# Kernel optimization log

Hardware: AMD Instinct MI355X
Metric: run time of the kernel (lower is better)

The kernel has to match this reference:

```python
import jax, jax.numpy as jnp
import numpy as np
from jax import lax

B, L, E = 16, 100, 128
NQ, NC, DL = 1000, 100, 100
NODE, PATH, MAXC = 5000, 5000, 128


def setup_inputs() -> dict:
    key = jax.random.key(0)
    ks = jax.random.split(key, 40)
    rn = lambda k, *s: jax.random.normal(k, s, jnp.float32) * 0.02
    inp = {}
    inp['code'] = jax.random.randint(ks[0], (B, L, NQ * 2 + MAXC * 3), 0, NODE, jnp.int32)
    inp['q'] = jax.random.randint(ks[1], (B, L), 0, NQ, jnp.int32)
    inp['c'] = jax.random.randint(ks[2], (B, L), 0, NC, jnp.int32)
    inp['sd'] = jax.random.randint(ks[3], (B, L), 0, DL, jnp.int32)
    inp['qd'] = jax.random.randint(ks[4], (B, L), 0, DL, jnp.int32)
    inp['a'] = jax.random.randint(ks[5], (B, L), 0, NQ * 2, jnp.int32)
    inp['qshft'] = jax.random.randint(ks[6], (B, L), 0, NQ, jnp.int32)
    inp['cshft'] = jax.random.randint(ks[7], (B, L), 0, NC, jnp.int32)
    inp['sdshft'] = jax.random.randint(ks[8], (B, L), 0, DL, jnp.int32)
    inp['qdshft'] = jax.random.randint(ks[9], (B, L), 0, DL, jnp.int32)
    # embedding tables (padding rows zeroed, matching torch padding_idx)
    inp['embed_nodes'] = rn(ks[10], NODE + 2, E)
    inp['embed_paths'] = rn(ks[11], PATH + 2, E)
    inp['q_tab'] = rn(ks[12], NQ + 1, E).at[NQ].set(0.0)
    inp['c_tab'] = rn(ks[13], NC + 1, E).at[NC].set(0.0)
    inp['sd_tab'] = rn(ks[14], DL + 100, E).at[0].set(0.0)
    inp['qd_tab'] = rn(ks[15], DL + 100, E).at[0].set(0.0)
    inp['a_tab'] = rn(ks[16], NQ * 2 + 2, E).at[2].set(0.0)
    inp['knowledge'] = rn(ks[17], 1, E)
    # linear weights stored [in, out] so y = x @ W + b
    inp['Wpt'] = rn(ks[18], 3 * E, 3 * E); inp['bpt'] = rn(ks[19], 3 * E)
    inp['Wat'] = rn(ks[20], 3 * E, 1);     inp['bat'] = rn(ks[21], 1)
    inp['Wqa'] = rn(ks[22], 4 * E, E);     inp['bqa'] = rn(ks[23], E)
    inp['W1'] = rn(ks[24], 4 * E, E);      inp['b1'] = rn(ks[25], E)
    inp['W2'] = rn(ks[26], E, E);          inp['b2'] = rn(ks[27], E)
    inp['W3'] = rn(ks[28], E, E);          inp['b3'] = rn(ks[29], E)
    inp['W4'] = rn(ks[30], 2 * E, E);      inp['b4'] = rn(ks[31], E)
    inp['W5'] = rn(ks[32], 2 * E, E);      inp['b5'] = rn(ks[33], E)
    inp['W6'] = rn(ks[34], 4 * E, E);      inp['b6'] = rn(ks[35], E)
    inp['Wf'] = rn(ks[36], E, 10);         inp['bf'] = rn(ks[37], 10)
    return inp


def reference(code, q, c, sd, qd, a, qshft, cshft, sdshft, qdshft,
              embed_nodes, embed_paths, q_tab, c_tab, sd_tab, qd_tab, a_tab,
              knowledge, Wpt, bpt, Wat, bat, Wqa, bqa, W1, b1, W2, b2, W3, b3,
              W4, b4, W5, b5, W6, b6, Wf, bf):
    Bq, Lq = q.shape
    # ---- code2vec attention over AST paths ----
    c2v = code[:, :, NQ * 2:].reshape(Bq, Lq, MAXC, 3)
    full = jnp.concatenate([embed_nodes[c2v[..., 0]],
                            embed_nodes[c2v[..., 2]],
                            embed_paths[c2v[..., 1]]], axis=-1)  # [B,L,MAXC,3E]
    tr = jnp.tanh(full @ Wpt + bpt)
    ctx = tr @ Wat + bat                      # [B,L,MAXC,1]
    attn = jax.nn.softmax(ctx, axis=1)        # softmax over seq dim (dim=1), as in source
    code_vec = jnp.sum(full * attn, axis=2)   # [B,L,3E]
    # ---- embeddings + input projections ----
    a_e = a_tab[a]
    acode = jnp.concatenate([a_e, code_vec], axis=-1) @ Wqa + bqa   # [B,L,E]
    inp = jnp.concatenate([q_tab[q], c_tab[c], sd_tab[sd], qd_tab[qd]], axis=-1) @ W1 + b1
    sd_e = sd_tab[sd]
    qd_e = qd_tab[qd]
    # ---- sequential SDF/PKA/KSU recurrence ----
    k0 = jnp.tile(knowledge, (Bq, 1))  # [B,E]

    def step(k, ts):
        inp_t, a_t, sd_t, qd_t = ts
        qq = inp_t - k
        sdf = jax.nn.sigmoid(qq @ W2 + b2) * jnp.tanh(qq @ W3 + b3)
        x = jnp.concatenate([sdf, a_t], axis=-1)
        pka = jax.nn.sigmoid(x @ W4 + b4) * jnp.tanh(x @ W5 + b5)
        ins = jnp.concatenate([k, a_t, sd_t, qd_t], axis=-1)
        g = jax.nn.sigmoid(ins @ W6 + b6)
        k_new = g * k + (1.0 - g) * pka
        return k_new, k_new @ Wf + bf

    xs = (inp.transpose(1, 0, 2), acode.transpose(1, 0, 2),
          sd_e.transpose(1, 0, 2), qd_e.transpose(1, 0, 2))
    _, logits = lax.scan(step, k0, xs)        # [L,B,10]
    return jax.nn.sigmoid(logits.transpose(1, 0, 2))  # [B,L,10]
```

## Files before the change

kernel.cpp:

```cpp
#include <hip/hip_runtime.h>
#include <hip/hip_bf16.h>

#define B_   16
#define L_   100
#define E_   128
#define NQ_  1000
#define MAXC_ 128
#define CODE_STRIDE (NQ_*2 + MAXC_*3)
#define CODE_OFF    (NQ_*2)
#define NROWS (B_*L_*MAXC_)

typedef short bf16x8 __attribute__((ext_vector_type(8)));
typedef float f32x4  __attribute__((ext_vector_type(4)));

__device__ __forceinline__ unsigned short f2b(float f) {
    unsigned u = __float_as_uint(f);
    unsigned r = (u + 0x7fffu + ((u >> 16) & 1u)) >> 16;
    return (unsigned short)r;
}
__device__ __forceinline__ unsigned cvt2(float lo, float hi) {
    unsigned r;
    asm("v_cvt_pk_bf16_f32 %0, %1, %2" : "=v"(r) : "v"(lo), "v"(hi));
    return r;
}
__device__ __forceinline__ float fsig(float x) {
    return __builtin_amdgcn_rcpf(1.0f + __builtin_amdgcn_exp2f(-1.44269504f * x));
}
__device__ __forceinline__ float ftanh(float x) {
    return 1.0f - 2.0f * __builtin_amdgcn_rcpf(1.0f + __builtin_amdgcn_exp2f(2.88539008f * x));
}
__device__ __forceinline__ void ldsbar() {
    asm volatile("s_waitcnt lgkmcnt(0)" ::: "memory");
    __builtin_amdgcn_s_barrier();
}
__device__ __forceinline__ void vmbar() {
    asm volatile("s_waitcnt vmcnt(0) lgkmcnt(0)" ::: "memory");
    __builtin_amdgcn_s_barrier();
}
__device__ __forceinline__ void gll16(const void* g, void* l) {
    __builtin_amdgcn_global_load_lds(
        (const __attribute__((address_space(1))) unsigned int*)g,
        (__attribute__((address_space(3))) unsigned int*)l, 16, 0, 0);
}

#define P0 576
#define P1 (P0+2501)
#define P2 (P1+2501)
#define P3 (P2+192)
#define P4 (P3+128)
#define P5 (P4+8)
#define P6 (P5+512)
#define P7 (P6+256)
#define P8 (P7+192)
#define P9 (P8+8)

__global__ void k_prep(const float* __restrict__ Wpt, const float* __restrict__ en,
                       const float* __restrict__ ep,
                       const float* __restrict__ W2, const float* __restrict__ W3,
                       const float* __restrict__ W4, const float* __restrict__ W5,
                       const float* __restrict__ W6, const float* __restrict__ Wf,
                       const float* __restrict__ Wqa, const float* __restrict__ W1,
                       unsigned short* __restrict__ wptT, unsigned short* __restrict__ enb,
                       unsigned short* __restrict__ epb, unsigned short* __restrict__ bt1,
                       unsigned short* __restrict__ bt2, unsigned short* __restrict__ btf,
                       unsigned short* __restrict__ bW1, unsigned short* __restrict__ bW2,
                       unsigned short* __restrict__ bW6, float* __restrict__ ssum)
{
    int blk = blockIdx.x;
    if (blk < P0) {
        int i = blk * 256 + threadIdx.x;
        if (i < 384*384) {
            int e = i & 7, G = i >> 3;
            int l15g = G & 15, rest = G >> 4;
            int l4g = rest & 3, rest2 = rest >> 2;
            int ksg = rest2 % 12, tile = rest2 / 12;
            int n = tile*16 + l15g, k = ksg*32 + l4g*8 + e;
            wptT[i] = f2b(Wpt[k*384 + n]);
        }
    } else if (blk < P1) {
        int i = (blk - P0) * 256 + threadIdx.x;
        if (i < 5002*128) enb[i] = f2b(en[i]);
    } else if (blk < P2) {
        int i = (blk - P1) * 256 + threadIdx.x;
        if (i < 5002*128) epb[i] = f2b(ep[i]);
    } else if (blk < P3) {
        int i = (blk - P2) * 256 + threadIdx.x;
        int n = i >> 7, k = i & 127;
        float v = (n < 128) ? W2[k*128 + n] : (n < 256) ? W3[k*128 + (n-128)]
                                                        : W6[k*128 + (n-256)];
        bt1[i] = f2b(v);
    } else if (blk < P4) {
        int i = (blk - P3) * 256 + threadIdx.x;
        int n = i >> 7, k = i & 127;
        float v = (n < 128) ? W4[k*128 + n] : W5[k*128 + (n-128)];
        bt2[i] = f2b(v);
    } else if (blk < P5) {
        int i = (blk - P4) * 256 + threadIdx.x;
        int n = i >> 7, k = i & 127;
        btf[i] = f2b(n < 10 ? Wf[k*10 + n] : 0.0f);
    } else if (blk < P6) {
        int i = (blk - P5) * 256 + threadIdx.x;
        int n = i >> 9, k = i & 511;
        float v = (n < 128) ? Wqa[k*128 + n] : W1[k*128 + (n-128)];
        bW1[i] = f2b(v);
    } else if (blk < P7) {
        int i = (blk - P6) * 256 + threadIdx.x;
        int n = i >> 7, k = i & 127;
        float v = (n < 128) ? W2[k*128 + n]
                : (n < 256) ? W3[k*128 + (n-128)]
                : (n < 384) ? W4[(128 + k)*128 + (n-256)]
                            : W5[(128 + k)*128 + (n-384)];
        bW2[i] = f2b(v);
    } else if (blk < P8) {
        int i = (blk - P7) * 256 + threadIdx.x;
        if (i < 128*384) {
            int n = i / 384, k = i % 384;
            bW6[i] = f2b(W6[(128 + k)*128 + n]);
        }
    } else {
        int i = (blk - P8) * 256 + threadIdx.x;
        if (i < B_ * MAXC_) ssum[i] = 0.0f;
    }
}

__global__ __launch_bounds__(256, 2) void k_ctx(const int* __restrict__ code,
    const unsigned short* __restrict__ enb, const unsigned short* __restrict__ epb,
    const unsigned short* __restrict__ wptT, const float* __restrict__ bpt,
    const float* __restrict__ wat, const float* __restrict__ bat,
    float* __restrict__ ectx, float* __restrict__ ssum)
{
    __shared__ __align__(16) unsigned short Bs[2][18432];
    __shared__ float bw[768];
    const int tid = threadIdx.x, wv = tid >> 6, lane = tid & 63;
    const int l15 = lane & 15, l4 = lane >> 4;
    const int rowg0 = blockIdx.x * 192;

    for (int idx = tid; idx < 768; idx += 256)
        bw[idx] = (idx < 384) ? bpt[idx] : wat[idx - 384];

    bf16x8 af[3][12];
    #pragma unroll
    for (int h = 0; h < 3; ++h) {
        int rowg = rowg0 + h * 64 + wv * 16 + l15;
        int rowc = (rowg < NROWS) ? rowg : (NROWS - 1);
        int m = rowc & 127, bl = rowc >> 7;
        const int* cp = code + (size_t)bl * CODE_STRIDE + CODE_OFF + m * 3;
        int i0 = cp[0], i1 = cp[1], i2 = cp[2];
        #pragma unroll
        for (int ks = 0; ks < 12; ++ks) {
            int seg = ks >> 2;
            int idx = (seg == 0) ? i0 : (seg == 1 ? i2 : i1);
            const unsigned short* tab = (seg == 2) ? epb : enb;
            af[h][ks] = *(const bf16x8*)(tab + (size_t)idx * 128 + (ks & 3) * 32 + l4 * 8);
        }
    }

    {
        const unsigned short* src = wptT;
        #pragma unroll
        for (int i = 0; i < 9; ++i) {
            int g0 = wv * 64 + i * 256;
            gll16(src + (size_t)g0 * 8 + lane * 8, &Bs[0][g0 * 8]);
        }
    }

    float cr[3][4] = {{0,0,0,0},{0,0,0,0},{0,0,0,0}};
    const float bat0 = bat[0];

    for (int nc = 0; nc < 8; ++nc) {
        vmbar();
        if (nc < 7) {
            const unsigned short* src = wptT + (size_t)(nc + 1) * 18432;
            #pragma unroll
            for (int i = 0; i < 9; ++i) {
                int g0 = wv * 64 + i * 256;
                gll16(src + (size_t)g0 * 8 + lane * 8, &Bs[(nc + 1) & 1][g0 * 8]);
            }
        }
        const char* bb = (const char*)&Bs[nc & 1][0] + l15 * 16;
        f32x4 acc[3][3] = {{{0,0,0,0},{0,0,0,0},{0,0,0,0}},
                           {{0,0,0,0},{0,0,0,0},{0,0,0,0}},
                           {{0,0,0,0},{0,0,0,0},{0,0,0,0}}};
        #pragma unroll
        for (int ks = 0; ks < 12; ++ks) {
            int go = (ks * 4 + l4) * 256;
            bf16x8 b0 = *(const bf16x8*)(bb + go);
            bf16x8 b1 = *(const bf16x8*)(bb + 24576 + go);
            bf16x8 b2 = *(const bf16x8*)(bb + 49152 + go);
            #pragma unroll
            for (int h = 0; h < 3; ++h) {
                acc[h][0] = __builtin_amdgcn_mfma_f32_16x16x32_bf16(af[h][ks], b0, acc[h][0], 0, 0, 0);
                acc[h][1] = __builtin_amdgcn_mfma_f32_16x16x32_bf16(af[h][ks], b1, acc[h][1], 0, 0, 0);
                acc[h][2] = __builtin_amdgcn_mfma_f32_16x16x32_bf16(af[h][ks], b2, acc[h][2], 0, 0, 0);
            }
        }
        #pragma unroll
        for (int tt = 0; tt < 3; ++tt) {
            int ng = nc * 48 + tt * 16 + l15;
            float bv = bw[ng], wa = bw[384 + ng];
            #pragma unroll
            for (int h = 0; h < 3; ++h)
                #pragma unroll
                for (int r = 0; r < 4; ++r)
                    cr[h][r] += ftanh(acc[h][tt][r] + bv) * wa;
        }
    }

    #pragma unroll
    for (int h = 0; h < 3; ++h)
        #pragma unroll
        for (int r = 0; r < 4; ++r) {
            float v = cr[h][r];
            v += __shfl_xor(v, 1); v += __shfl_xor(v, 2);
            v += __shfl_xor(v, 4); v += __shfl_xor(v, 8);
            cr[h][r] = v;
        }
    if (l15 == 0) {
        #pragma unroll
        for (int h = 0; h < 3; ++h) {
            int rbase = rowg0 + h * 64 + wv * 16 + l4 * 4;
            #pragma unroll
            for (int r = 0; r < 4; ++r) {
                int row = rbase + r;
                if (row < NROWS) {
                    float e = __builtin_amdgcn_exp2f((cr[h][r] + bat0) * 1.44269504f);
                    ectx[row] = e;
                    int bl = row >> 7, m = row & 127;
                    atomicAdd(&ssum[(bl / 100) * 128 + m], e);
                }
            }
        }
    }
}

__global__ __launch_bounds__(192) void k_codevec(const int* __restrict__ code,
    const float* __restrict__ ectx, const float* __restrict__ ssum,
    const unsigned short* __restrict__ enb, const unsigned short* __restrict__ epb,
    float* __restrict__ cv)
{
    __shared__ float sm[128];
    int bl = blockIdx.x;
    int t = threadIdx.x;
    if (t < 128) {
        sm[t] = ectx[(size_t)bl * MAXC_ + t]
                * __builtin_amdgcn_rcpf(ssum[(bl / 100) * 128 + t]);
    }
    ldsbar();
    int seg = t >> 6, tc = t & 63;
    const int* cp = code + (size_t)bl * CODE_STRIDE + CODE_OFF;
    const unsigned short* tab = (seg == 2) ? epb : enb;
    const int sidx = (seg == 0) ? 0 : (seg == 1) ? 2 : 1;
    float ax = 0.f, ay = 0.f;
    #pragma unroll 8
    for (int m = 0; m < MAXC_; ++m) {
        float w = sm[m];
        int idx = cp[m * 3 + sidx];
        unsigned u = *((const unsigned*)(tab + (size_t)idx * 128) + tc);
        ax += w * __uint_as_float(u << 16);
        ay += w * __uint_as_float(u & 0xffff0000u);
    }
    float2 o; o.x = ax; o.y = ay;
    *(float2*)(cv + (size_t)bl * 384 + seg * 128 + tc * 2) = o;
}

__global__ __launch_bounds__(256) void k_fuse(
    const int* __restrict__ a, const int* __restrict__ q, const int* __restrict__ c,
    const int* __restrict__ sd, const int* __restrict__ qd,
    const float* __restrict__ a_tab, const float* __restrict__ q_tab,
    const float* __restrict__ c_tab, const float* __restrict__ sd_tab,
    const float* __restrict__ qd_tab, const float* __restrict__ cv,
    const unsigned short* __restrict__ bW1, const unsigned short* __restrict__ bW2,
    const unsigned short* __restrict__ bW6,
    const float* __restrict__ bqa, const float* __restrict__ b1,
    const float* __restrict__ b2, const float* __restrict__ b3,
    const float* __restrict__ b4, const float* __restrict__ b5,
    const float* __restrict__ b6,
    float4* __restrict__ preQ, float* __restrict__ pre6)
{
    __shared__ __align__(16) unsigned short X[16 * 1024];
    __shared__ __align__(16) unsigned short Y[16 * 256];
    const int tid = threadIdx.x, wv = tid >> 6, lane = tid & 63;
    const int l15 = lane & 15, l4 = lane >> 4;
    const int row0 = blockIdx.x * 16;

    #pragma unroll
    for (int it = 0; it < 16; ++it) {
        int idx = tid + it * 256;
        int r = idx >> 8, col = (idx & 255) * 4;
        int row = row0 + r;
        const float* src;
        if (col < 128)       src = a_tab + (size_t)a[row] * 128 + col;
        else if (col < 512)  src = cv + (size_t)row * 384 + (col - 128);
        else if (col < 640)  src = q_tab + (size_t)q[row] * 128 + (col - 512);
        else if (col < 768)  src = c_tab + (size_t)c[row] * 128 + (col - 640);
        else if (col < 896)  src = sd_tab + (size_t)sd[row] * 128 + (col - 768);
        else                 src = qd_tab + (size_t)qd[row] * 128 + (col - 896);
        float4 v = *(const float4*)src;
        unsigned u0 = cvt2(v.x, v.y), u1 = cvt2(v.z, v.w);
        int byte = r * 2048 + ((((col >> 3)) ^ (r & 7)) << 4) + ((col & 4) << 1);
        *(unsigned*)((char*)X + byte) = u0;
        *(unsigned*)((char*)X + byte + 4) = u1;
    }
    ldsbar();

    {
        bf16x8 ak[16];
        int kbase = (wv < 2) ? 0 : 512;
        #pragma unroll
        for (int ks = 0; ks < 16; ++ks) {
            int col = kbase + ks * 32 + l4 * 8;
            ak[ks] = *(const bf16x8*)((const char*)X + l15 * 2048 + (((col >> 3) ^ (l15 & 7)) << 4));
        }
        int nbase = wv * 64;
        f32x4 acc[4] = {{0,0,0,0},{0,0,0,0},{0,0,0,0},{0,0,0,0}};
        #pragma unroll
        for (int i = 0; i < 4; ++i) {
            const unsigned short* bp = bW1 + (size_t)(nbase + i * 16 + l15) * 512 + l4 * 8;
            #pragma unroll
            for (int ks = 0; ks < 16; ++ks) {
                bf16x8 bfr = *(const bf16x8*)(bp + ks * 32);
                acc[i] = __builtin_amdgcn_mfma_f32_16x16x32_bf16(ak[ks], bfr, acc[i], 0, 0, 0);
            }
        }
        #pragma unroll
        for (int i = 0; i < 4; ++i) {
            int cc = nbase + i * 16 + l15;
            float bias = (cc < 128) ? bqa[cc] : b1[cc - 128];
            #pragma unroll
            for (int rr = 0; rr < 4; ++rr) {
                int row = l4 * 4 + rr;
                int byte = row * 512 + (((cc >> 3) ^ (row & 7)) << 4) + (cc & 7) * 2;
                *(unsigned short*)((char*)Y + byte) = f2b(acc[i][rr] + bias);
            }
        }
    }
    ldsbar();

    bf16x8 zi[4], za[4], zs[4], zq[4];
    #pragma unroll
    for (int ks = 0; ks < 4; ++ks) {
        int ci = 128 + ks * 32 + l4 * 8;
        zi[ks] = *(const bf16x8*)((const char*)Y + l15 * 512 + (((ci >> 3) ^ (l15 & 7)) << 4));
        int ca = ks * 32 + l4 * 8;
        za[ks] = *(const bf16x8*)((const char*)Y + l15 * 512 + (((ca >> 3) ^ (l15 & 7)) << 4));
        int cs = 768 + ks * 32 + l4 * 8;
        zs[ks] = *(const bf16x8*)((const char*)X + l15 * 2048 + (((cs >> 3) ^ (l15 & 7)) << 4));
        int cq = 896 + ks * 32 + l4 * 8;
        zq[ks] = *(const bf16x8*)((const char*)X + l15 * 2048 + (((cq >> 3) ^ (l15 & 7)) << 4));
    }
    f32x4 A2[2] = {{0,0,0,0},{0,0,0,0}}, A3[2] = {{0,0,0,0},{0,0,0,0}};
    f32x4 A4[2] = {{0,0,0,0},{0,0,0,0}}, A5[2] = {{0,0,0,0},{0,0,0,0}};
    f32x4 A6[2] = {{0,0,0,0},{0,0,0,0}};
    #pragma unroll
    for (int tt = 0; tt < 2; ++tt) {
        int n = wv * 32 + tt * 16 + l15;
        const unsigned short* p2 = bW2 + (size_t)(      n) * 128 + l4 * 8;
        const unsigned short* p3 = bW2 + (size_t)(128 + n) * 128 + l4 * 8;
        const unsigned short* p4 = bW2 + (size_t)(256 + n) * 128 + l4 * 8;
        const unsigned short* p5 = bW2 + (size_t)(384 + n) * 128 + l4 * 8;
        const unsigned short* p6 = bW6 + (size_t)n * 384 + l4 * 8;
        #pragma unroll
        for (int ks = 0; ks < 4; ++ks) {
            A2[tt] = __builtin_amdgcn_mfma_f32_16x16x32_bf16(zi[ks], *(const bf16x8*)(p2 + ks*32), A2[tt], 0, 0, 0);
            A3[tt] = __builtin_amdgcn_mfma_f32_16x16x32_bf16(zi[ks], *(const bf16x8*)(p3 + ks*32), A3[tt], 0, 0, 0);
            A4[tt] = __builtin_amdgcn_mfma_f32_16x16x32_bf16(za[ks], *(const bf16x8*)(p4 + ks*32), A4[tt], 0, 0, 0);
            A5[tt] = __builtin_amdgcn_mfma_f32_16x16x32_bf16(za[ks], *(const bf16x8*)(p5 + ks*32), A5[tt], 0, 0, 0);
            A6[tt] = __builtin_amdgcn_mfma_f32_16x16x32_bf16(za[ks], *(const bf16x8*)(p6 + ks*32), A6[tt], 0, 0, 0);
        }
        #pragma unroll
        for (int ks = 0; ks < 4; ++ks)
            A6[tt] = __builtin_amdgcn_mfma_f32_16x16x32_bf16(zs[ks], *(const bf16x8*)(p6 + 256 + ks*32), A6[tt], 0, 0, 0);
        #pragma unroll
        for (int ks = 0; ks < 4; ++ks)
            A6[tt] = __builtin_amdgcn_mfma_f32_16x16x32_bf16(zq[ks], *(const bf16x8*)(p6 + 512 + ks*32), A6[tt], 0, 0, 0);
    }
    #pragma unroll
    for (int tt = 0; tt < 2; ++tt) {
        int n = wv * 32 + tt * 16 + l15;
        float c2 = b2[n], c3 = b3[n], c4 = b4[n], c5 = b5[n], c6 = b6[n];
        #pragma unroll
        for (int rr = 0; rr < 4; ++rr) {
            size_t row = (size_t)(row0 + l4 * 4 + rr);
            float4 o;
            o.x = A2[tt][rr] + c2; o.y = A3[tt][rr] + c3;
            o.z = A4[tt][rr] + c4; o.w = A5[tt][rr] + c5;
            preQ[row * 128 + n] = o;
            pre6[row * 128 + n] = A6[tt][rr] + c6;
        }
    }
}

__global__ __launch_bounds__(512) void k_recur(
    const unsigned short* __restrict__ bt1, const unsigned short* __restrict__ bt2,
    const float* __restrict__ knowledge, const float4* __restrict__ preQ,
    const float* __restrict__ pre6, unsigned short* __restrict__ khist)
{
    __shared__ __align__(16) unsigned short k_lds[16 * 128];
    __shared__ __align__(16) unsigned short s_lds[16 * 128];
    const int tid = threadIdx.x, wv = tid >> 6, lane = tid & 63;
    const int l15 = lane & 15, l4 = lane >> 4;
    const int j = wv * 16 + l15;

    bf16x8 w2f[4], w3f[4], w6f[4], w4f[4], w5f[4];
    #pragma unroll
    for (int ks = 0; ks < 4; ++ks) {
        w2f[ks] = *(const bf16x8*)(bt1 + (size_t)(      j) * 128 + ks * 32 + l4 * 8);
        w3f[ks] = *(const bf16x8*)(bt1 + (size_t)(128 + j) * 128 + ks * 32 + l4 * 8);
        w6f[ks] = *(const bf16x8*)(bt1 + (size_t)(256 + j) * 128 + ks * 32 + l4 * 8);
        w4f[ks] = *(const bf16x8*)(bt2 + (size_t)(      j) * 128 + ks * 32 + l4 * 8);
        w5f[ks] = *(const bf16x8*)(bt2 + (size_t)(128 + j) * 128 + ks * 32 + l4 * 8);
    }

    float kreg[4], gR[4];
    {
        float k0 = knowledge[j];
        unsigned short kb = f2b(k0);
        #pragma unroll
        for (int r = 0; r < 4; ++r) {
            kreg[r] = k0;
            int b = l4 * 4 + r;
            k_lds[b * 128 + (((j >> 3) ^ b) << 3) + (j & 7)] = kb;
        }
    }
    ldsbar();

    float4 pv[4]; float p6[4];
    #pragma unroll
    for (int r = 0; r < 4; ++r) {
        int b = l4 * 4 + r;
        size_t ix = (size_t)(b * L_) * 128 + j;
        pv[r] = preQ[ix]; p6[r] = pre6[ix];
    }

    for (int t = 0; t < L_; ++t) {
        float4 pvN[4]; float p6N[4];
        #pragma unroll
        for (int r = 0; r < 4; ++r) {
            int b = l4 * 4 + r;
            size_t ix = (size_t)(b * L_ + t + 1) * 128 + j;
            pvN[r] = preQ[ix]; p6N[r] = pre6[ix];
        }

        bf16x8 ak[4];
        {
            const unsigned short* kb = k_lds + l15 * 128;
            #pragma unroll
            for (int ks = 0; ks < 4; ++ks)
                ak[ks] = *(const bf16x8*)(kb + (((ks * 4 + l4) ^ l15) << 3));
        }
        f32x4 a2 = {0,0,0,0}, a3 = {0,0,0,0}, a6 = {0,0,0,0};
        #pragma unroll
        for (int ks = 0; ks < 4; ++ks) {
            a2 = __builtin_amdgcn_mfma_f32_16x16x32_bf16(ak[ks], w2f[ks], a2, 0, 0, 0);
            a3 = __builtin_amdgcn_mfma_f32_16x16x32_bf16(ak[ks], w3f[ks], a3, 0, 0, 0);
            a6 = __builtin_amdgcn_mfma_f32_16x16x32_bf16(ak[ks], w6f[ks], a6, 0, 0, 0);
        }
        #pragma unroll
        for (int r = 0; r < 4; ++r) {
            int b = l4 * 4 + r;
            float sdf = fsig(pv[r].x - a2[r]) * ftanh(pv[r].y - a3[r]);
            gR[r] = fsig(a6[r] + p6[r]);
            s_lds[b * 128 + (((j >> 3) ^ b) << 3) + (j & 7)] = f2b(sdf);
        }
        ldsbar();
        bf16x8 as[4];
        {
            const unsigned short* sb = s_lds + l15 * 128;
            #pragma unroll
            for (int ks = 0; ks < 4; ++ks)
                as[ks] = *(const bf16x8*)(sb + (((ks * 4 + l4) ^ l15) << 3));
        }
        f32x4 a4 = {0,0,0,0}, a5 = {0,0,0,0};
        #pragma unroll
        for (int ks = 0; ks < 4; ++ks) {
            a4 = __builtin_amdgcn_mfma_f32_16x16x32_bf16(as[ks], w4f[ks], a4, 0, 0, 0);
            a5 = __builtin_amdgcn_mfma_f32_16x16x32_bf16(as[ks], w5f[ks], a5, 0, 0, 0);
        }
        #pragma unroll
        for (int r = 0; r < 4; ++r) {
            int b = l4 * 4 + r;
            float pka = fsig(a4[r] + pv[r].z) * ftanh(a5[r] + pv[r].w);
            float kn = gR[r] * kreg[r] + (1.0f - gR[r]) * pka;
            kreg[r] = kn;
            unsigned short kb2 = f2b(kn);
            k_lds[b * 128 + (((j >> 3) ^ b) << 3) + (j & 7)] = kb2;
            khist[(size_t)(b * L_ + t) * 128 + j] = kb2;
        }
        #pragma unroll
        for (int r = 0; r < 4; ++r) { pv[r] = pvN[r]; p6[r] = p6N[r]; }
        ldsbar();
    }
}

__global__ __launch_bounds__(256) void k_logits(const unsigned short* __restrict__ khist,
    const unsigned short* __restrict__ btf, const float* __restrict__ bfv,
    float* __restrict__ out)
{
    int wv = threadIdx.x >> 6, lane = threadIdx.x & 63;
    int l15 = lane & 15, l4 = lane >> 4;
    int R0 = (blockIdx.x * 4 + wv) * 16;
    bf16x8 wbf[4], akr[4];
    #pragma unroll
    for (int ks = 0; ks < 4; ++ks)
        wbf[ks] = *(const bf16x8*)(btf + (size_t)l15 * 128 + ks * 32 + l4 * 8);
    const unsigned short* kb = khist + (size_t)(R0 + l15) * 128;
    #pragma unroll
    for (int ks = 0; ks < 4; ++ks)
        akr[ks] = *(const bf16x8*)(kb + ks * 32 + l4 * 8);
    f32x4 af = {0.f, 0.f, 0.f, 0.f};
    #pragma unroll
    for (int ks = 0; ks < 4; ++ks)
        af = __builtin_amdgcn_mfma_f32_16x16x32_bf16(akr[ks], wbf[ks], af, 0, 0, 0);
    if (l15 < 10) {
        float bb = bfv[l15];
        #pragma unroll
        for (int r = 0; r < 4; ++r)
            out[(size_t)(R0 + l4 * 4 + r) * 10 + l15] = fsig(af[r] + bb);
    }
}

extern "C" void kernel_launch(void* const* d_in, const int* in_sizes, int n_in,
                              void* d_out, int out_size, void* d_ws, size_t ws_size,
                              hipStream_t stream)
{
    const int*   code  = (const int*)d_in[0];
    const int*   q     = (const int*)d_in[1];
    const int*   c     = (const int*)d_in[2];
    const int*   sd    = (const int*)d_in[3];
    const int*   qd    = (const int*)d_in[4];
    const int*   a     = (const int*)d_in[5];
    const float* en    = (const float*)d_in[10];
    const float* ep    = (const float*)d_in[11];
    const float* q_tab = (const float*)d_in[12];
    const float* c_tab = (const float*)d_in[13];
    const float* sd_tab= (const float*)d_in[14];
    const float* qd_tab= (const float*)d_in[15];
    const float* a_tab = (const float*)d_in[16];
    const float* know  = (const float*)d_in[17];
    const float* Wpt   = (const float*)d_in[18];
    const float* bpt   = (const float*)d_in[19];
    const float* Wat   = (const float*)d_in[20];
    const float* bat   = (const float*)d_in[21];
    const float* Wqa   = (const float*)d_in[22];
    const float* bqa   = (const float*)d_in[23];
    const float* W1    = (const float*)d_in[24];
    const float* b1    = (const float*)d_in[25];
    const float* W2    = (const float*)d_in[26];
    const float* b2    = (const float*)d_in[27];
    const float* W3    = (const float*)d_in[28];
    const float* b3    = (const float*)d_in[29];
    const float* W4    = (const float*)d_in[30];
    const float* b4    = (const float*)d_in[31];
    const float* W5    = (const float*)d_in[32];
    const float* b5    = (const float*)d_in[33];
    const float* W6    = (const float*)d_in[34];
    const float* b6    = (const float*)d_in[35];
    const float* Wf    = (const float*)d_in[36];
    const float* bf_   = (const float*)d_in[37];

    char* ws = (char*)d_ws;
    size_t off = 0;
    auto alloc = [&](size_t n) { size_t r = off; off += (n + 255) & ~(size_t)255; return r; };
    unsigned short* wptT = (unsigned short*)(ws + alloc(384 * 384 * 2));
    unsigned short* enb  = (unsigned short*)(ws + alloc(5002 * 128 * 2));
    unsigned short* epb  = (unsigned short*)(ws + alloc(5002 * 128 * 2));
    unsigned short* bt1  = (unsigned short*)(ws + alloc(384 * 128 * 2));
    unsigned short* bt2  = (unsigned short*)(ws + alloc(256 * 128 * 2));
    unsigned short* btf  = (unsigned short*)(ws + alloc(16 * 128 * 2));
    unsigned short* bW1  = (unsigned short*)(ws + alloc(256 * 512 * 2));
    unsigned short* bW2  = (unsigned short*)(ws + alloc(512 * 128 * 2));
    unsigned short* bW6  = (unsigned short*)(ws + alloc(128 * 384 * 2));
    float* ectx  = (float*)(ws + alloc((size_t)NROWS * 4));
    float* ssum  = (float*)(ws + alloc((size_t)B_ * MAXC_ * 4));
    float* cv    = (float*)(ws + alloc((size_t)B_ * L_ * 384 * 4));
    float4* preQ = (float4*)(ws + alloc(((size_t)B_ * L_ * 128 + 128) * 16));
    float* pre6  = (float*)(ws + alloc(((size_t)B_ * L_ * 128 + 128) * 4));
    unsigned short* khist = (unsigned short*)(ws + alloc((size_t)B_ * L_ * 128 * 2));
    float* outf  = (float*)d_out;

    k_prep<<<P9, 256, 0, stream>>>(Wpt, en, ep, W2, W3, W4, W5, W6, Wf,
                                   Wqa, W1,
                                   wptT, enb, epb, bt1, bt2, btf,
                                   bW1, bW2, bW6, ssum);
    k_ctx<<<1067, 256, 0, stream>>>(code, enb, epb, wptT, bpt, Wat, bat, ectx, ssum);
    k_codevec<<<1600, 192, 0, stream>>>(code, ectx, ssum, enb, epb, cv);
    k_fuse<<<100, 256, 0, stream>>>(a, q, c, sd, qd, a_tab, q_tab, c_tab, sd_tab,
                                    qd_tab, cv, bW1, bW2, bW6, bqa, b1,
                                    b2, b3, b4, b5, b6, preQ, pre6);
    k_recur<<<1, 512, 0, stream>>>(bt1, bt2, know, preQ, pre6, khist);
    k_logits<<<25, 256, 0, stream>>>(khist, btf, bf_, outf);
}
```

Before: 280.9 us.

## Read Wpt B-fragments directly from global in k_ctx, shrink row tile

The k_ctx attention-score kernel drops its LDS double-buffered staging of the transposed Wpt weights (global_load_lds plus barriers) and instead loads B fragments straight from global memory/L2 per MFMA step. The per-block row tile shrinks from 192 to 128 rows (2 row groups per wave instead of 3), so the grid becomes 1600 blocks that divide NROWS exactly, and the bounds checks go away. This removes LDS traffic and barriers and frees LDS for higher occupancy, at the cost of more redundant global/L2 weight reads per block and less reuse of each B fragment.

```diff
diff --git a/kernel.cpp b/kernel.cpp
--- a/kernel.cpp
+++ b/kernel.cpp
@@ -32,15 +32,6 @@
 __device__ __forceinline__ void ldsbar() {
     asm volatile("s_waitcnt lgkmcnt(0)" ::: "memory");
     __builtin_amdgcn_s_barrier();
-}
-__device__ __forceinline__ void vmbar() {
-    asm volatile("s_waitcnt vmcnt(0) lgkmcnt(0)" ::: "memory");
-    __builtin_amdgcn_s_barrier();
-}
-__device__ __forceinline__ void gll16(const void* g, void* l) {
-    __builtin_amdgcn_global_load_lds(
-        (const __attribute__((address_space(1))) unsigned int*)g,
-        (__attribute__((address_space(3))) unsigned int*)l, 16, 0, 0);
 }
 
 #define P0 576
@@ -123,27 +114,21 @@
     }
 }
 
-__global__ __launch_bounds__(256, 2) void k_ctx(const int* __restrict__ code,
+__global__ __launch_bounds__(256) void k_ctx(const int* __restrict__ code,
     const unsigned short* __restrict__ enb, const unsigned short* __restrict__ epb,
     const unsigned short* __restrict__ wptT, const float* __restrict__ bpt,
     const float* __restrict__ wat, const float* __restrict__ bat,
     float* __restrict__ ectx, float* __restrict__ ssum)
 {
-    __shared__ __align__(16) unsigned short Bs[2][18432];
-    __shared__ float bw[768];
     const int tid = threadIdx.x, wv = tid >> 6, lane = tid & 63;
     const int l15 = lane & 15, l4 = lane >> 4;
-    const int rowg0 = blockIdx.x * 192;
-
-    for (int idx = tid; idx < 768; idx += 256)
-        bw[idx] = (idx < 384) ? bpt[idx] : wat[idx - 384];
-
-    bf16x8 af[3][12];
-    #pragma unroll
-    for (int h = 0; h < 3; ++h) {
+    const int rowg0 = blockIdx.x * 128;
+
+    bf16x8 af[2][12];
+    #pragma unroll
+    for (int h = 0; h < 2; ++h) {
         int rowg = rowg0 + h * 64 + wv * 16 + l15;
-        int rowc = (rowg < NROWS) ? rowg : (NROWS - 1);
-        int m = rowc & 127, bl = rowc >> 7;
+        int m = rowg & 127, bl = rowg >> 7;
         const int* cp = code + (size_t)bl * CODE_STRIDE + CODE_OFF + m * 3;
         int i0 = cp[0], i1 = cp[1], i2 = cp[2];
         #pragma unroll
@@ -155,59 +140,30 @@
         }
     }
 
-    {
-        const unsigned short* src = wptT;
-        #pragma unroll
-        for (int i = 0; i < 9; ++i) {
-            int g0 = wv * 64 + i * 256;
-            gll16(src + (size_t)g0 * 8 + lane * 8, &Bs[0][g0 * 8]);
-        }
-    }
-
-    float cr[3][4] = {{0,0,0,0},{0,0,0,0},{0,0,0,0}};
+    float cr[2][4] = {{0.f,0.f,0.f,0.f},{0.f,0.f,0.f,0.f}};
     const float bat0 = bat[0];
-
-    for (int nc = 0; nc < 8; ++nc) {
-        vmbar();
-        if (nc < 7) {
-            const unsigned short* src = wptT + (size_t)(nc + 1) * 18432;
-            #pragma unroll
-            for (int i = 0; i < 9; ++i) {
-                int g0 = wv * 64 + i * 256;
-                gll16(src + (size_t)g0 * 8 + lane * 8, &Bs[(nc + 1) & 1][g0 * 8]);
-            }
-        }
-        const char* bb = (const char*)&Bs[nc & 1][0] + l15 * 16;
-        f32x4 acc[3][3] = {{{0,0,0,0},{0,0,0,0},{0,0,0,0}},
-                           {{0,0,0,0},{0,0,0,0},{0,0,0,0}},
-                           {{0,0,0,0},{0,0,0,0},{0,0,0,0}}};
+    const unsigned short* bbase = wptT + l4 * 128 + l15 * 8;
+
+    for (int t = 0; t < 24; ++t) {
+        const unsigned short* bp = bbase + t * 6144;
+        f32x4 acc0 = {0.f,0.f,0.f,0.f}, acc1 = {0.f,0.f,0.f,0.f};
         #pragma unroll
         for (int ks = 0; ks < 12; ++ks) {
-            int go = (ks * 4 + l4) * 256;
-            bf16x8 b0 = *(const bf16x8*)(bb + go);
-            bf16x8 b1 = *(const bf16x8*)(bb + 24576 + go);
-            bf16x8 b2 = *(const bf16x8*)(bb + 49152 + go);
-            #pragma unroll
-            for (int h = 0; h < 3; ++h) {
-                acc[h][0] = __builtin_amdgcn_mfma_f32_16x16x32_bf16(af[h][ks], b0, acc[h][0], 0, 0, 0);
-                acc[h][1] = __builtin_amdgcn_mfma_f32_16x16x32_bf16(af[h][ks], b1, acc[h][1], 0, 0, 0);
-                acc[h][2] = __builtin_amdgcn_mfma_f32_16x16x32_bf16(af[h][ks], b2, acc[h][2], 0, 0, 0);
-            }
-        }
-        #pragma unroll
-        for (int tt = 0; tt < 3; ++tt) {
-            int ng = nc * 48 + tt * 16 + l15;
-            float bv = bw[ng], wa = bw[384 + ng];
-            #pragma unroll
-            for (int h = 0; h < 3; ++h)
-                #pragma unroll
-                for (int r = 0; r < 4; ++r)
-                    cr[h][r] += ftanh(acc[h][tt][r] + bv) * wa;
-        }
-    }
-
-    #pragma unroll
-    for (int h = 0; h < 3; ++h)
+            bf16x8 b0 = *(const bf16x8*)(bp + ks * 512);
+            acc0 = __builtin_amdgcn_mfma_f32_16x16x32_bf16(af[0][ks], b0, acc0, 0, 0, 0);
+            acc1 = __builtin_amdgcn_mfma_f32_16x16x32_bf16(af[1][ks], b0, acc1, 0, 0, 0);
+        }
+        int ng = t * 16 + l15;
+        float bv = bpt[ng], wa = wat[ng];
+        #pragma unroll
+        for (int r = 0; r < 4; ++r) {
+            cr[0][r] += ftanh(acc0[r] + bv) * wa;
+            cr[1][r] += ftanh(acc1[r] + bv) * wa;
+        }
+    }
+
+    #pragma unroll
+    for (int h = 0; h < 2; ++h)
         #pragma unroll
         for (int r = 0; r < 4; ++r) {
             float v = cr[h][r];
@@ -217,17 +173,15 @@
         }
     if (l15 == 0) {
         #pragma unroll
-        for (int h = 0; h < 3; ++h) {
+        for (int h = 0; h < 2; ++h) {
             int rbase = rowg0 + h * 64 + wv * 16 + l4 * 4;
             #pragma unroll
             for (int r = 0; r < 4; ++r) {
                 int row = rbase + r;
-                if (row < NROWS) {
-                    float e = __builtin_amdgcn_exp2f((cr[h][r] + bat0) * 1.44269504f);
-                    ectx[row] = e;
-                    int bl = row >> 7, m = row & 127;
-                    atomicAdd(&ssum[(bl / 100) * 128 + m], e);
-                }
+                float e = __builtin_amdgcn_exp2f((cr[h][r] + bat0) * 1.44269504f);
+                ectx[row] = e;
+                int bl = row >> 7, m = row & 127;
+                atomicAdd(&ssum[(bl / 100) * 128 + m], e);
             }
         }
     }
@@ -582,7 +536,7 @@
                                    Wqa, W1,
                                    wptT, enb, epb, bt1, bt2, btf,
                                    bW1, bW2, bW6, ssum);
-    k_ctx<<<1067, 256, 0, stream>>>(code, enb, epb, wptT, bpt, Wat, bat, ectx, ssum);
+    k_ctx<<<1600, 256, 0, stream>>>(code, enb, epb, wptT, bpt, Wat, bat, ectx, ssum);
     k_codevec<<<1600, 192, 0, stream>>>(code, ectx, ssum, enb, epb, cv);
     k_fuse<<<100, 256, 0, stream>>>(a, q, c, sd, qd, a_tab, q_tab, c_tab, sd_tab,
                                     qd_tab, cv, bW1, bW2, bW6, bqa, b1,
```

After: 314.9 us. 12.1% more time.
